# Optimization experiments

Measured on AMD Instinct MI355X. Metric: run time of the kernel, lower is better.

The kernel has to match this reference:

```python
import jax, jax.numpy as jnp
import numpy as np

TOP_K = 2
NORM_MIN = 1e-12
B, S, H = 2, 1024, 2048
E, I = 16, 1024
SHARED_I = 2048  # moe_intermediate_size * moe_num_shared_experts


def setup_inputs() -> dict:
    key = jax.random.key(0)
    ks = jax.random.split(key, 8)
    s = 0.02  # init scale
    return {
        "hidden_states": jax.random.normal(ks[0], (B, S, H), jnp.float32),
        "router_w": jax.random.normal(ks[1], (E, H), jnp.float32) * s,
        "w_gate": jax.random.normal(ks[2], (E, H, I), jnp.float32) * s,
        "w_up": jax.random.normal(ks[3], (E, H, I), jnp.float32) * s,
        "w_down": jax.random.normal(ks[4], (E, I, H), jnp.float32) * s,
        "ws_gate": jax.random.normal(ks[5], (H, SHARED_I), jnp.float32) * s,
        "ws_up": jax.random.normal(ks[6], (H, SHARED_I), jnp.float32) * s,
        "ws_down": jax.random.normal(ks[7], (SHARED_I, H), jnp.float32) * s,
    }


def reference(hidden_states, router_w, w_gate, w_up, w_down, ws_gate, ws_up, ws_down):
    b, s, h = hidden_states.shape
    x = hidden_states.reshape(-1, h)                      # [N, H]
    n = x.shape[0]

    # Router: float32 softmax -> top-k -> renormalize with clamp
    router_logits = x.astype(jnp.float32) @ router_w.T    # [N, E]
    probs = jax.nn.softmax(router_logits, axis=-1)
    rw, sel = jax.lax.top_k(probs, TOP_K)                 # [N, K]
    rw = rw / jnp.clip(rw.sum(axis=-1, keepdims=True), NORM_MIN)
    rw = rw.astype(x.dtype)

    # Dense combine weights [N, E] (equivalent to one_hot dispatch/scatter)
    combine = jnp.zeros((n, E), x.dtype).at[jnp.arange(n)[:, None], sel].set(rw)

    # All-expert SwiGLU MLP (full-capacity MoE, no dropped tokens)
    g = jnp.einsum('nh,ehi->eni', x, w_gate)              # [E, N, I]
    u = jnp.einsum('nh,ehi->eni', x, w_up)
    o = jnp.einsum('eni,eih->enh', jax.nn.silu(g) * u, w_down)  # [E, N, H]
    out = jnp.einsum('enh,ne->nh', o, combine)            # weighted combine

    # Shared expert path
    shared = (jax.nn.silu(x @ ws_gate) * (x @ ws_up)) @ ws_down
    out = out + shared

    return out.reshape(b, s, h), router_logits
```

## Files before the change

### kernel.cpp

```cpp
#include <hip/hip_runtime.h>
#include <cstdint>
#include <cstddef>
#include <cmath>

#define N_TOK 2048
#define HDIM  2048
#define NEXP  16
#define IDIM  1024
#define SIDIM 2048
#define NTHREADS 256

typedef __attribute__((ext_vector_type(8))) short bf16x8;
typedef __attribute__((ext_vector_type(4))) float f32x4;

__device__ __forceinline__ uint32_t f2bf_u(float f) {
    union { float f; uint32_t u; } v; v.f = f;
    return (v.u + 0x7FFFu + ((v.u >> 16) & 1u)) >> 16;
}
__device__ __forceinline__ uint32_t pack2bf(float lo, float hi) {
    return f2bf_u(lo) | (f2bf_u(hi) << 16);
}

__device__ __forceinline__ int swz(int row, int c) {
    return row * 4 + (c ^ ((row >> 1) & 3));
}

__global__ __launch_bounds__(NTHREADS)
void convert_x_kernel(const float* __restrict__ x, unsigned short* __restrict__ xb)
{
    const size_t i = ((size_t)blockIdx.x * NTHREADS + threadIdx.x) * 8;
    float4 a = *(const float4*)(x + i);
    float4 b = *(const float4*)(x + i + 4);
    uint4 w = make_uint4(pack2bf(a.x, a.y), pack2bf(a.z, a.w),
                         pack2bf(b.x, b.y), pack2bf(b.z, b.w));
    *(uint4*)(xb + i) = w;
}

__global__ __launch_bounds__(NTHREADS)
void router_kernel(const float* __restrict__ x,
                   const float* __restrict__ rw,
                   float* __restrict__ logits_out,
                   int* __restrict__ cnt,
                   int* __restrict__ tok_list,
                   float* __restrict__ wt_list)
{
    const int n = blockIdx.x;
    const int tid = threadIdx.x;
    const float* xr = x + (size_t)n * HDIM;

    float acc[NEXP];
#pragma unroll
    for (int e = 0; e < NEXP; ++e) acc[e] = 0.f;

    for (int h = tid; h < HDIM; h += NTHREADS) {
        float xv = xr[h];
#pragma unroll
        for (int e = 0; e < NEXP; ++e) acc[e] += xv * rw[(size_t)e * HDIM + h];
    }

    __shared__ float red[NEXP][NTHREADS];
#pragma unroll
    for (int e = 0; e < NEXP; ++e) red[e][tid] = acc[e];
    __syncthreads();
    for (int s = NTHREADS / 2; s > 0; s >>= 1) {
        if (tid < s) {
#pragma unroll
            for (int e = 0; e < NEXP; ++e) red[e][tid] += red[e][tid + s];
        }
        __syncthreads();
    }

    if (tid < NEXP) logits_out[(size_t)n * NEXP + tid] = red[tid][0];

    if (tid == 0) {
        float l[NEXP];
#pragma unroll
        for (int e = 0; e < NEXP; ++e) l[e] = red[e][0];
        int e0 = 0;
#pragma unroll
        for (int e = 1; e < NEXP; ++e) if (l[e] > l[e0]) e0 = e;
        int e1 = (e0 == 0) ? 1 : 0;
#pragma unroll
        for (int e = 0; e < NEXP; ++e)
            if (e != e0 && l[e] > l[e1]) e1 = e;
        float t = expf(l[e1] - l[e0]);
        float s = 1.f + t;
        float rw0 = 1.f / s;
        float rw1 = t / s;
        int p0 = atomicAdd(&cnt[e0], 1);
        tok_list[e0 * N_TOK + p0] = n;
        wt_list[e0 * N_TOK + p0] = rw0;
        int p1 = atomicAdd(&cnt[e1], 1);
        tok_list[e1 * N_TOK + p1] = n;
        wt_list[e1 * N_TOK + p1] = rw1;
    }
}

__global__ void prefix_kernel(const int* __restrict__ cnt, int* __restrict__ base)
{
    if (threadIdx.x == 0) {
        int s = 0;
        for (int e = 0; e < NEXP; ++e) { base[e] = s; s += cnt[e]; }
    }
}

__global__ __launch_bounds__(NTHREADS)
void dual_swiglu_mfma(const unsigned short* __restrict__ Xb,
                      const float* __restrict__ WgAll,
                      const float* __restrict__ WuAll,
                      unsigned short* __restrict__ Y,
                      const int* __restrict__ cnt,
                      const int* __restrict__ base,
                      const int* __restrict__ tok_list,
                      const int Icols)
{
    const int e  = blockIdx.z;
    const int m0 = blockIdx.y * 128;
    const int n0 = blockIdx.x * 64;
    const bool gathered = (tok_list != nullptr);
    const int M = gathered ? cnt[e] : N_TOK;
    if (m0 >= M) return;
    const float* Wg = WgAll + (size_t)e * HDIM * Icols;
    const float* Wu = WuAll + (size_t)e * HDIM * Icols;
    const int yb = gathered ? base[e] : 0;

    __shared__ short As[128 * 32];
    __shared__ short Gs[64 * 32];
    __shared__ short Us[64 * 32];

    const int tid  = threadIdx.x;
    const int lane = tid & 63;
    const int wave = tid >> 6;
    const int wm   = wave >> 1;
    const int wn   = wave & 1;
    const int l15  = lane & 15;
    const int q    = lane >> 4;

    const int ar = tid >> 1;
    const int at = tid & 1;
    const int slotA = m0 + ar;
    int xrow;
    if (gathered) xrow = tok_list[e * N_TOK + ((slotA < M) ? slotA : (M - 1))];
    else          xrow = slotA;
    const unsigned short* xp = Xb + (size_t)xrow * HDIM + at * 16;

    const int wcn = tid & 63;
    const int wcc = tid >> 6;
    const float* gp = Wg + n0 + wcn;
    const float* up = Wu + n0 + wcn;

    f32x4 accg[4][2], accu[4][2];
#pragma unroll
    for (int i = 0; i < 4; ++i)
#pragma unroll
        for (int j = 0; j < 2; ++j) {
            accg[i][j] = (f32x4){0.f, 0.f, 0.f, 0.f};
            accu[i][j] = (f32x4){0.f, 0.f, 0.f, 0.f};
        }

    uint4 a0, a1;
    float g8[8], u8[8];
    auto ldtile = [&](int kk) {
        a0 = *(const uint4*)(xp + kk);
        a1 = *(const uint4*)(xp + kk + 8);
#pragma unroll
        for (int j = 0; j < 8; ++j) {
            g8[j] = gp[(size_t)(kk + wcc * 8 + j) * Icols];
            u8[j] = up[(size_t)(kk + wcc * 8 + j) * Icols];
        }
    };

    ldtile(0);
    for (int k0 = 0; k0 < HDIM; k0 += 32) {
        __syncthreads();
        *(uint4*)(As + swz(ar, at * 2 + 0) * 8) = a0;
        *(uint4*)(As + swz(ar, at * 2 + 1) * 8) = a1;
        uint4 gw = make_uint4(pack2bf(g8[0], g8[1]), pack2bf(g8[2], g8[3]),
                              pack2bf(g8[4], g8[5]), pack2bf(g8[6], g8[7]));
        uint4 uw = make_uint4(pack2bf(u8[0], u8[1]), pack2bf(u8[2], u8[3]),
                              pack2bf(u8[4], u8[5]), pack2bf(u8[6], u8[7]));
        *(uint4*)(Gs + swz(wcn, wcc) * 8) = gw;
        *(uint4*)(Us + swz(wcn, wcc) * 8) = uw;
        __syncthreads();

        int kn = k0 + 32;
        if (kn >= HDIM) kn = k0;
        ldtile(kn);

        bf16x8 af[4], bg[2], bu[2];
#pragma unroll
        for (int i = 0; i < 4; ++i)
            af[i] = *(const bf16x8*)(As + swz(wm * 64 + i * 16 + l15, q) * 8);
#pragma unroll
        for (int j = 0; j < 2; ++j) {
            bg[j] = *(const bf16x8*)(Gs + swz(wn * 32 + j * 16 + l15, q) * 8);
            bu[j] = *(const bf16x8*)(Us + swz(wn * 32 + j * 16 + l15, q) * 8);
        }
#pragma unroll
        for (int i = 0; i < 4; ++i)
#pragma unroll
            for (int j = 0; j < 2; ++j) {
                accg[i][j] = __builtin_amdgcn_mfma_f32_16x16x32_bf16(af[i], bg[j], accg[i][j], 0, 0, 0);
                accu[i][j] = __builtin_amdgcn_mfma_f32_16x16x32_bf16(af[i], bu[j], accu[i][j], 0, 0, 0);
            }
    }

#pragma unroll
    for (int i = 0; i < 4; ++i) {
#pragma unroll
        for (int r = 0; r < 4; ++r) {
            const int slot = m0 + wm * 64 + i * 16 + q * 4 + r;
            if (slot < M) {
                unsigned short* yrow = Y + (size_t)(yb + slot) * Icols;
#pragma unroll
                for (int j = 0; j < 2; ++j) {
                    const int col = n0 + wn * 32 + j * 16 + l15;
                    float g = accg[i][j][r];
                    float u = accu[i][j][r];
                    float y = (g / (1.f + expf(-g))) * u;
                    yrow[col] = (unsigned short)f2bf_u(y);
                }
            }
        }
    }
}

__global__ __launch_bounds__(NTHREADS)
void down_mfma(const unsigned short* __restrict__ A,
               const float* __restrict__ WdAll,
               float* __restrict__ out,
               const int* __restrict__ cnt,
               const int* __restrict__ base,
               const int* __restrict__ tok_list,
               const float* __restrict__ wt_list,
               const int K)
{
    const int e  = blockIdx.z;
    const int m0 = blockIdx.y * 64;
    const int n0 = blockIdx.x * 128;
    const bool scatter = (tok_list != nullptr);
    const int M = scatter ? cnt[e] : N_TOK;
    if (m0 >= M) return;
    const float* Wd = WdAll + (size_t)e * K * HDIM;
    const int yb = scatter ? base[e] : 0;

    __shared__ short As[64 * 32];
    __shared__ short Bs[128 * 32];

    const int tid  = threadIdx.x;
    const int lane = tid & 63;
    const int wave = tid >> 6;
    const int wm   = wave >> 1;
    const int wn   = wave & 1;
    const int l15  = lane & 15;
    const int q    = lane >> 4;

    const int ar = tid >> 2;
    const int ac = tid & 3;
    const int slotA = m0 + ar;
    const int arow = yb + ((slotA < M) ? slotA : (M - 1));
    const unsigned short* ap = A + (size_t)arow * K + ac * 8;

    const int bn = tid & 127;
    const int bh = tid >> 7;
    const float* bp = Wd + n0 + bn;

    f32x4 acc[2][4];
#pragma unroll
    for (int i = 0; i < 2; ++i)
#pragma unroll
        for (int j = 0; j < 4; ++j) acc[i][j] = (f32x4){0.f, 0.f, 0.f, 0.f};

    uint4 a0;
    float b16[16];
    auto ldtile = [&](int kk) {
        a0 = *(const uint4*)(ap + kk);
#pragma unroll
        for (int c = 0; c < 2; ++c)
#pragma unroll
            for (int j = 0; j < 8; ++j)
                b16[c * 8 + j] = bp[(size_t)(kk + (bh * 2 + c) * 8 + j) * HDIM];
    };

    ldtile(0);
    for (int k0 = 0; k0 < K; k0 += 32) {
        __syncthreads();
        *(uint4*)(As + swz(ar, ac) * 8) = a0;
        uint4 w0 = make_uint4(pack2bf(b16[0], b16[1]), pack2bf(b16[2], b16[3]),
                              pack2bf(b16[4], b16[5]), pack2bf(b16[6], b16[7]));
        uint4 w1 = make_uint4(pack2bf(b16[8], b16[9]), pack2bf(b16[10], b16[11]),
                              pack2bf(b16[12], b16[13]), pack2bf(b16[14], b16[15]));
        *(uint4*)(Bs + swz(bn, bh * 2 + 0) * 8) = w0;
        *(uint4*)(Bs + swz(bn, bh * 2 + 1) * 8) = w1;
        __syncthreads();

        int kn = k0 + 32;
        if (kn >= K) kn = k0;
        ldtile(kn);

        bf16x8 af[2], bfr[4];
#pragma unroll
        for (int i = 0; i < 2; ++i)
            af[i] = *(const bf16x8*)(As + swz(wm * 32 + i * 16 + l15, q) * 8);
#pragma unroll
        for (int j = 0; j < 4; ++j)
            bfr[j] = *(const bf16x8*)(Bs + swz(wn * 64 + j * 16 + l15, q) * 8);
#pragma unroll
        for (int i = 0; i < 2; ++i)
#pragma unroll
            for (int j = 0; j < 4; ++j)
                acc[i][j] = __builtin_amdgcn_mfma_f32_16x16x32_bf16(af[i], bfr[j], acc[i][j], 0, 0, 0);
    }

#pragma unroll
    for (int i = 0; i < 2; ++i) {
#pragma unroll
        for (int r = 0; r < 4; ++r) {
            const int slot = m0 + wm * 32 + i * 16 + q * 4 + r;
            if (slot >= M) continue;
            if (scatter) {
                const int tok = tok_list[e * N_TOK + slot];
                const float wt = wt_list[e * N_TOK + slot];
                float* orow = out + (size_t)tok * HDIM;
#pragma unroll
                for (int j = 0; j < 4; ++j) {
                    const int col = n0 + wn * 64 + j * 16 + l15;
                    atomicAdd(&orow[col], wt * acc[i][j][r]);
                }
            } else {
                float* orow = out + (size_t)slot * HDIM;
#pragma unroll
                for (int j = 0; j < 4; ++j) {
                    const int col = n0 + wn * 64 + j * 16 + l15;
                    orow[col] = acc[i][j][r];
                }
            }
        }
    }
}

extern "C" void kernel_launch(void* const* d_in, const int* in_sizes, int n_in,
                              void* d_out, int out_size, void* d_ws, size_t ws_size,
                              hipStream_t stream)
{
    const float* x       = (const float*)d_in[0];
    const float* rw      = (const float*)d_in[1];
    const float* w_gate  = (const float*)d_in[2];
    const float* w_up    = (const float*)d_in[3];
    const float* w_down  = (const float*)d_in[4];
    const float* ws_gate = (const float*)d_in[5];
    const float* ws_up   = (const float*)d_in[6];
    const float* ws_down = (const float*)d_in[7];

    float* out    = (float*)d_out;
    float* logits = out + (size_t)N_TOK * HDIM;

    char* w = (char*)d_ws;
    int* cnt      = (int*)w;
    int* base     = cnt + 16;
    int* tok_list = base + 16;
    float* wt_list = (float*)(tok_list + NEXP * N_TOK);
    uintptr_t p = (uintptr_t)(wt_list + NEXP * N_TOK);
    p = (p + 255) & ~(uintptr_t)255;
    unsigned short* Xb       = (unsigned short*)p;
    unsigned short* A_shared = Xb + (size_t)N_TOK * HDIM;
    unsigned short* Ybuf     = A_shared + (size_t)N_TOK * SIDIM;

    hipMemsetAsync(cnt, 0, 16 * sizeof(int), stream);

    convert_x_kernel<<<dim3((N_TOK * HDIM) / (NTHREADS * 8)), dim3(NTHREADS), 0, stream>>>(x, Xb);
    router_kernel<<<dim3(N_TOK), dim3(NTHREADS), 0, stream>>>(
        x, rw, logits, cnt, tok_list, wt_list);
    prefix_kernel<<<dim3(1), dim3(64), 0, stream>>>(cnt, base);

    dual_swiglu_mfma<<<dim3(SIDIM / 64, N_TOK / 128, 1), dim3(NTHREADS), 0, stream>>>(
        Xb, ws_gate, ws_up, A_shared, cnt, base, nullptr, SIDIM);
    down_mfma<<<dim3(HDIM / 128, N_TOK / 64, 1), dim3(NTHREADS), 0, stream>>>(
        A_shared, ws_down, out, cnt, base, nullptr, nullptr, SIDIM);

    dual_swiglu_mfma<<<dim3(IDIM / 64, N_TOK / 128, NEXP), dim3(NTHREADS), 0, stream>>>(
        Xb, w_gate, w_up, Ybuf, cnt, base, tok_list, IDIM);
    down_mfma<<<dim3(HDIM / 128, N_TOK / 64, NEXP), dim3(NTHREADS), 0, stream>>>(
        Ybuf, w_down, out, cnt, base, tok_list, wt_list, IDIM);
}
```

Measured before the change: 713.2 us.

## Double-buffer LDS tiles with one barrier per step and hardware bf16 pack

Both the gate/up and down GEMM kernels now keep two LDS buffers and two register tiles. Each k-step issues the global load for the next tile before storing the current one, so there is one barrier per 32-wide k-step instead of two. Float-to-bf16 packing switches from software rounding to the v_cvt_pk_bf16_f32 instruction. The cost is doubled shared memory and more registers, which may reduce occupancy, and the barrier relies on manual waitcnt and sched_barrier ordering.

Measured after the change: 766.3 us. 1.07x slower.

```diff
diff --git a/kernel.cpp b/kernel.cpp
--- a/kernel.cpp
+++ b/kernel.cpp
@@ -17,8 +17,11 @@
     union { float f; uint32_t u; } v; v.f = f;
     return (v.u + 0x7FFFu + ((v.u >> 16) & 1u)) >> 16;
 }
-__device__ __forceinline__ uint32_t pack2bf(float lo, float hi) {
-    return f2bf_u(lo) | (f2bf_u(hi) << 16);
+
+__device__ __forceinline__ uint32_t cvtpk(float lo, float hi) {
+    uint32_t r;
+    asm("v_cvt_pk_bf16_f32 %0, %1, %2" : "=v"(r) : "v"(lo), "v"(hi));
+    return r;
 }
 
 __device__ __forceinline__ int swz(int row, int c) {
@@ -31,8 +34,8 @@
     const size_t i = ((size_t)blockIdx.x * NTHREADS + threadIdx.x) * 8;
     float4 a = *(const float4*)(x + i);
     float4 b = *(const float4*)(x + i + 4);
-    uint4 w = make_uint4(pack2bf(a.x, a.y), pack2bf(a.z, a.w),
-                         pack2bf(b.x, b.y), pack2bf(b.z, b.w));
+    uint4 w = make_uint4(cvtpk(a.x, a.y), cvtpk(a.z, a.w),
+                         cvtpk(b.x, b.y), cvtpk(b.z, b.w));
     *(uint4*)(xb + i) = w;
 }
 
@@ -124,9 +127,9 @@
     const float* Wu = WuAll + (size_t)e * HDIM * Icols;
     const int yb = gathered ? base[e] : 0;
 
-    __shared__ short As[128 * 32];
-    __shared__ short Gs[64 * 32];
-    __shared__ short Us[64 * 32];
+    __shared__ short As[2][128 * 32];
+    __shared__ short Gs[2][64 * 32];
+    __shared__ short Us[2][64 * 32];
 
     const int tid  = threadIdx.x;
     const int lane = tid & 63;
@@ -158,43 +161,39 @@
             accu[i][j] = (f32x4){0.f, 0.f, 0.f, 0.f};
         }
 
-    uint4 a0, a1;
-    float g8[8], u8[8];
-    auto ldtile = [&](int kk) {
-        a0 = *(const uint4*)(xp + kk);
-        a1 = *(const uint4*)(xp + kk + 8);
+    struct RegTile { uint4 x0, x1; float g[8], u[8]; };
+    RegTile r0, r1;
+
+    auto ldtile = [&](RegTile& r, int kk) {
+        r.x0 = *(const uint4*)(xp + kk);
+        r.x1 = *(const uint4*)(xp + kk + 8);
+        const float* gk = gp + (size_t)(kk + wcc * 8) * Icols;
+        const float* uk = up + (size_t)(kk + wcc * 8) * Icols;
 #pragma unroll
         for (int j = 0; j < 8; ++j) {
-            g8[j] = gp[(size_t)(kk + wcc * 8 + j) * Icols];
-            u8[j] = up[(size_t)(kk + wcc * 8 + j) * Icols];
-        }
-    };
-
-    ldtile(0);
-    for (int k0 = 0; k0 < HDIM; k0 += 32) {
-        __syncthreads();
-        *(uint4*)(As + swz(ar, at * 2 + 0) * 8) = a0;
-        *(uint4*)(As + swz(ar, at * 2 + 1) * 8) = a1;
-        uint4 gw = make_uint4(pack2bf(g8[0], g8[1]), pack2bf(g8[2], g8[3]),
-                              pack2bf(g8[4], g8[5]), pack2bf(g8[6], g8[7]));
-        uint4 uw = make_uint4(pack2bf(u8[0], u8[1]), pack2bf(u8[2], u8[3]),
-                              pack2bf(u8[4], u8[5]), pack2bf(u8[6], u8[7]));
-        *(uint4*)(Gs + swz(wcn, wcc) * 8) = gw;
-        *(uint4*)(Us + swz(wcn, wcc) * 8) = uw;
-        __syncthreads();
-
-        int kn = k0 + 32;
-        if (kn >= HDIM) kn = k0;
-        ldtile(kn);
-
+            r.g[j] = gk[(size_t)j * Icols];
+            r.u[j] = uk[(size_t)j * Icols];
+        }
+    };
+    auto sttile = [&](const RegTile& r, short* As_, short* Gs_, short* Us_) {
+        *(uint4*)(As_ + swz(ar, at * 2 + 0) * 8) = r.x0;
+        *(uint4*)(As_ + swz(ar, at * 2 + 1) * 8) = r.x1;
+        uint4 gw = make_uint4(cvtpk(r.g[0], r.g[1]), cvtpk(r.g[2], r.g[3]),
+                              cvtpk(r.g[4], r.g[5]), cvtpk(r.g[6], r.g[7]));
+        uint4 uw = make_uint4(cvtpk(r.u[0], r.u[1]), cvtpk(r.u[2], r.u[3]),
+                              cvtpk(r.u[4], r.u[5]), cvtpk(r.u[6], r.u[7]));
+        *(uint4*)(Gs_ + swz(wcn, wcc) * 8) = gw;
+        *(uint4*)(Us_ + swz(wcn, wcc) * 8) = uw;
+    };
+    auto mmstep = [&](const short* As_, const short* Gs_, const short* Us_) {
         bf16x8 af[4], bg[2], bu[2];
 #pragma unroll
         for (int i = 0; i < 4; ++i)
-            af[i] = *(const bf16x8*)(As + swz(wm * 64 + i * 16 + l15, q) * 8);
+            af[i] = *(const bf16x8*)(As_ + swz(wm * 64 + i * 16 + l15, q) * 8);
 #pragma unroll
         for (int j = 0; j < 2; ++j) {
-            bg[j] = *(const bf16x8*)(Gs + swz(wn * 32 + j * 16 + l15, q) * 8);
-            bu[j] = *(const bf16x8*)(Us + swz(wn * 32 + j * 16 + l15, q) * 8);
+            bg[j] = *(const bf16x8*)(Gs_ + swz(wn * 32 + j * 16 + l15, q) * 8);
+            bu[j] = *(const bf16x8*)(Us_ + swz(wn * 32 + j * 16 + l15, q) * 8);
         }
 #pragma unroll
         for (int i = 0; i < 4; ++i)
@@ -203,6 +202,26 @@
                 accg[i][j] = __builtin_amdgcn_mfma_f32_16x16x32_bf16(af[i], bg[j], accg[i][j], 0, 0, 0);
                 accu[i][j] = __builtin_amdgcn_mfma_f32_16x16x32_bf16(af[i], bu[j], accu[i][j], 0, 0, 0);
             }
+    };
+
+    ldtile(r0, 0);
+    for (int k0 = 0; k0 < HDIM; k0 += 64) {
+        const int k1 = k0 + 32;
+        int k2 = k0 + 64; if (k2 >= HDIM) k2 = 0;
+
+        ldtile(r1, k1);
+        sttile(r0, As[0], Gs[0], Us[0]);
+        asm volatile("s_waitcnt lgkmcnt(0)" ::: "memory");
+        __builtin_amdgcn_s_barrier();
+        __builtin_amdgcn_sched_barrier(0);
+        mmstep(As[0], Gs[0], Us[0]);
+
+        ldtile(r0, k2);
+        sttile(r1, As[1], Gs[1], Us[1]);
+        asm volatile("s_waitcnt lgkmcnt(0)" ::: "memory");
+        __builtin_amdgcn_s_barrier();
+        __builtin_amdgcn_sched_barrier(0);
+        mmstep(As[1], Gs[1], Us[1]);
     }
 
 #pragma unroll
@@ -244,8 +263,8 @@
     const float* Wd = WdAll + (size_t)e * K * HDIM;
     const int yb = scatter ? base[e] : 0;
 
-    __shared__ short As[64 * 32];
-    __shared__ short Bs[128 * 32];
+    __shared__ short As[2][64 * 32];
+    __shared__ short Bs[2][128 * 32];
 
     const int tid  = threadIdx.x;
     const int lane = tid & 63;
@@ -271,45 +290,60 @@
 #pragma unroll
         for (int j = 0; j < 4; ++j) acc[i][j] = (f32x4){0.f, 0.f, 0.f, 0.f};
 
-    uint4 a0;
-    float b16[16];
-    auto ldtile = [&](int kk) {
-        a0 = *(const uint4*)(ap + kk);
+    struct RegTileD { uint4 x; float b[16]; };
+    RegTileD r0, r1;
+
+    auto ldtile = [&](RegTileD& r, int kk) {
+        r.x = *(const uint4*)(ap + kk);
+        const float* bk = bp + (size_t)(kk + bh * 16) * HDIM;
 #pragma unroll
         for (int c = 0; c < 2; ++c)
 #pragma unroll
             for (int j = 0; j < 8; ++j)
-                b16[c * 8 + j] = bp[(size_t)(kk + (bh * 2 + c) * 8 + j) * HDIM];
-    };
-
-    ldtile(0);
-    for (int k0 = 0; k0 < K; k0 += 32) {
-        __syncthreads();
-        *(uint4*)(As + swz(ar, ac) * 8) = a0;
-        uint4 w0 = make_uint4(pack2bf(b16[0], b16[1]), pack2bf(b16[2], b16[3]),
-                              pack2bf(b16[4], b16[5]), pack2bf(b16[6], b16[7]));
-        uint4 w1 = make_uint4(pack2bf(b16[8], b16[9]), pack2bf(b16[10], b16[11]),
-                              pack2bf(b16[12], b16[13]), pack2bf(b16[14], b16[15]));
-        *(uint4*)(Bs + swz(bn, bh * 2 + 0) * 8) = w0;
-        *(uint4*)(Bs + swz(bn, bh * 2 + 1) * 8) = w1;
-        __syncthreads();
-
-        int kn = k0 + 32;
-        if (kn >= K) kn = k0;
-        ldtile(kn);
-
+                r.b[c * 8 + j] = bk[(size_t)(c * 8 + j) * HDIM];
+    };
+    auto sttile = [&](const RegTileD& r, short* As_, short* Bs_) {
+        *(uint4*)(As_ + swz(ar, ac) * 8) = r.x;
+        uint4 w0 = make_uint4(cvtpk(r.b[0], r.b[1]),  cvtpk(r.b[2], r.b[3]),
+                              cvtpk(r.b[4], r.b[5]),  cvtpk(r.b[6], r.b[7]));
+        uint4 w1 = make_uint4(cvtpk(r.b[8], r.b[9]),  cvtpk(r.b[10], r.b[11]),
+                              cvtpk(r.b[12], r.b[13]), cvtpk(r.b[14], r.b[15]));
+        *(uint4*)(Bs_ + swz(bn, bh * 2 + 0) * 8) = w0;
+        *(uint4*)(Bs_ + swz(bn, bh * 2 + 1) * 8) = w1;
+    };
+    auto mmstep = [&](const short* As_, const short* Bs_) {
         bf16x8 af[2], bfr[4];
 #pragma unroll
         for (int i = 0; i < 2; ++i)
-            af[i] = *(const bf16x8*)(As + swz(wm * 32 + i * 16 + l15, q) * 8);
+            af[i] = *(const bf16x8*)(As_ + swz(wm * 32 + i * 16 + l15, q) * 8);
 #pragma unroll
         for (int j = 0; j < 4; ++j)
-            bfr[j] = *(const bf16x8*)(Bs + swz(wn * 64 + j * 16 + l15, q) * 8);
+            bfr[j] = *(const bf16x8*)(Bs_ + swz(wn * 64 + j * 16 + l15, q) * 8);
 #pragma unroll
         for (int i = 0; i < 2; ++i)
 #pragma unroll
             for (int j = 0; j < 4; ++j)
                 acc[i][j] = __builtin_amdgcn_mfma_f32_16x16x32_bf16(af[i], bfr[j], acc[i][j], 0, 0, 0);
+    };
+
+    ldtile(r0, 0);
+    for (int k0 = 0; k0 < K; k0 += 64) {
+        const int k1 = k0 + 32;
+        int k2 = k0 + 64; if (k2 >= K) k2 = 0;
+
+        ldtile(r1, k1);
+        sttile(r0, As[0], Bs[0]);
+        asm volatile("s_waitcnt lgkmcnt(0)" ::: "memory");
+        __builtin_amdgcn_s_barrier();
+        __builtin_amdgcn_sched_barrier(0);
+        mmstep(As[0], Bs[0]);
+
+        ldtile(r0, k2);
+        sttile(r1, As[1], Bs[1]);
+        asm volatile("s_waitcnt lgkmcnt(0)" ::: "memory");
+        __builtin_amdgcn_s_barrier();
+        __builtin_amdgcn_sched_barrier(0);
+        mmstep(As[1], Bs[1]);
     }
 
 #pragma unroll
```

## Merge shared and routed expert GEMMs into single launches; use hardware bf16 pack

Applied to the files above, without the earlier changes.

Folds the shared-expert GEMMs into the routed-expert launches as an extra z-slice, so the up/gate and down stages each run as one grid instead of two. The down stage now accumulates the shared path with atomics too, which requires zeroing the output with a memset first. Float-to-bf16 packing now uses the v_cvt_pk_bf16_f32 instruction instead of manual rounding. The aim is fewer launches, better GPU fill from the small sparse grids, and cheaper conversion. In exchange, the shared path pays atomic traffic and a full output memset, and many blocks exit early in the padded grid.

After: 756.4 us. 1.06x slower.

```diff
diff --git a/kernel.cpp b/kernel.cpp
--- a/kernel.cpp
+++ b/kernel.cpp
@@ -17,8 +17,11 @@
     union { float f; uint32_t u; } v; v.f = f;
     return (v.u + 0x7FFFu + ((v.u >> 16) & 1u)) >> 16;
 }
-__device__ __forceinline__ uint32_t pack2bf(float lo, float hi) {
-    return f2bf_u(lo) | (f2bf_u(hi) << 16);
+
+__device__ __forceinline__ uint32_t cvtpk(float lo, float hi) {
+    uint32_t r;
+    asm("v_cvt_pk_bf16_f32 %0, %1, %2" : "=v"(r) : "v"(lo), "v"(hi));
+    return r;
 }
 
 __device__ __forceinline__ int swz(int row, int c) {
@@ -31,8 +34,8 @@
     const size_t i = ((size_t)blockIdx.x * NTHREADS + threadIdx.x) * 8;
     float4 a = *(const float4*)(x + i);
     float4 b = *(const float4*)(x + i + 4);
-    uint4 w = make_uint4(pack2bf(a.x, a.y), pack2bf(a.z, a.w),
-                         pack2bf(b.x, b.y), pack2bf(b.z, b.w));
+    uint4 w = make_uint4(cvtpk(a.x, a.y), cvtpk(a.z, a.w),
+                         cvtpk(b.x, b.y), cvtpk(b.z, b.w));
     *(uint4*)(xb + i) = w;
 }
 
@@ -108,21 +111,27 @@
 void dual_swiglu_mfma(const unsigned short* __restrict__ Xb,
                       const float* __restrict__ WgAll,
                       const float* __restrict__ WuAll,
-                      unsigned short* __restrict__ Y,
+                      const float* __restrict__ Wsg,
+                      const float* __restrict__ Wsu,
+                      unsigned short* __restrict__ Ysparse,
+                      unsigned short* __restrict__ Yshared,
                       const int* __restrict__ cnt,
                       const int* __restrict__ base,
-                      const int* __restrict__ tok_list,
-                      const int Icols)
-{
-    const int e  = blockIdx.z;
+                      const int* __restrict__ tok_list)
+{
+    const int z  = blockIdx.z;
+    const bool shared_path = (z == 0);
+    const int e  = z - 1;
+    const int Icols = shared_path ? SIDIM : IDIM;
     const int m0 = blockIdx.y * 128;
     const int n0 = blockIdx.x * 64;
-    const bool gathered = (tok_list != nullptr);
-    const int M = gathered ? cnt[e] : N_TOK;
+    if (n0 >= Icols) return;
+    const int M = shared_path ? N_TOK : cnt[e];
     if (m0 >= M) return;
-    const float* Wg = WgAll + (size_t)e * HDIM * Icols;
-    const float* Wu = WuAll + (size_t)e * HDIM * Icols;
-    const int yb = gathered ? base[e] : 0;
+    const float* Wg = shared_path ? Wsg : WgAll + (size_t)e * HDIM * IDIM;
+    const float* Wu = shared_path ? Wsu : WuAll + (size_t)e * HDIM * IDIM;
+    unsigned short* Y = shared_path ? Yshared : Ysparse;
+    const int yb = shared_path ? 0 : base[e];
 
     __shared__ short As[128 * 32];
     __shared__ short Gs[64 * 32];
@@ -140,8 +149,8 @@
     const int at = tid & 1;
     const int slotA = m0 + ar;
     int xrow;
-    if (gathered) xrow = tok_list[e * N_TOK + ((slotA < M) ? slotA : (M - 1))];
-    else          xrow = slotA;
+    if (!shared_path) xrow = tok_list[e * N_TOK + ((slotA < M) ? slotA : (M - 1))];
+    else              xrow = slotA;
     const unsigned short* xp = Xb + (size_t)xrow * HDIM + at * 16;
 
     const int wcn = tid & 63;
@@ -175,10 +184,10 @@
         __syncthreads();
         *(uint4*)(As + swz(ar, at * 2 + 0) * 8) = a0;
         *(uint4*)(As + swz(ar, at * 2 + 1) * 8) = a1;
-        uint4 gw = make_uint4(pack2bf(g8[0], g8[1]), pack2bf(g8[2], g8[3]),
-                              pack2bf(g8[4], g8[5]), pack2bf(g8[6], g8[7]));
-        uint4 uw = make_uint4(pack2bf(u8[0], u8[1]), pack2bf(u8[2], u8[3]),
-                              pack2bf(u8[4], u8[5]), pack2bf(u8[6], u8[7]));
+        uint4 gw = make_uint4(cvtpk(g8[0], g8[1]), cvtpk(g8[2], g8[3]),
+                              cvtpk(g8[4], g8[5]), cvtpk(g8[6], g8[7]));
+        uint4 uw = make_uint4(cvtpk(u8[0], u8[1]), cvtpk(u8[2], u8[3]),
+                              cvtpk(u8[4], u8[5]), cvtpk(u8[6], u8[7]));
         *(uint4*)(Gs + swz(wcn, wcc) * 8) = gw;
         *(uint4*)(Us + swz(wcn, wcc) * 8) = uw;
         __syncthreads();
@@ -226,23 +235,27 @@
 }
 
 __global__ __launch_bounds__(NTHREADS)
-void down_mfma(const unsigned short* __restrict__ A,
+void down_mfma(const unsigned short* __restrict__ Ash,
+               const unsigned short* __restrict__ Asp,
+               const float* __restrict__ Wsd,
                const float* __restrict__ WdAll,
                float* __restrict__ out,
                const int* __restrict__ cnt,
                const int* __restrict__ base,
                const int* __restrict__ tok_list,
-               const float* __restrict__ wt_list,
-               const int K)
-{
-    const int e  = blockIdx.z;
+               const float* __restrict__ wt_list)
+{
+    const int z  = blockIdx.z;
+    const bool shared_path = (z == 0);
+    const int e  = z - 1;
+    const int K  = shared_path ? SIDIM : IDIM;
     const int m0 = blockIdx.y * 64;
     const int n0 = blockIdx.x * 128;
-    const bool scatter = (tok_list != nullptr);
-    const int M = scatter ? cnt[e] : N_TOK;
+    const int M = shared_path ? N_TOK : cnt[e];
     if (m0 >= M) return;
-    const float* Wd = WdAll + (size_t)e * K * HDIM;
-    const int yb = scatter ? base[e] : 0;
+    const unsigned short* A = shared_path ? Ash : Asp;
+    const float* Wd = shared_path ? Wsd : WdAll + (size_t)e * IDIM * HDIM;
+    const int yb = shared_path ? 0 : base[e];
 
     __shared__ short As[64 * 32];
     __shared__ short Bs[128 * 32];
@@ -286,10 +299,10 @@
     for (int k0 = 0; k0 < K; k0 += 32) {
         __syncthreads();
         *(uint4*)(As + swz(ar, ac) * 8) = a0;
-        uint4 w0 = make_uint4(pack2bf(b16[0], b16[1]), pack2bf(b16[2], b16[3]),
-                              pack2bf(b16[4], b16[5]), pack2bf(b16[6], b16[7]));
-        uint4 w1 = make_uint4(pack2bf(b16[8], b16[9]), pack2bf(b16[10], b16[11]),
-                              pack2bf(b16[12], b16[13]), pack2bf(b16[14], b16[15]));
+        uint4 w0 = make_uint4(cvtpk(b16[0], b16[1]),  cvtpk(b16[2], b16[3]),
+                              cvtpk(b16[4], b16[5]),  cvtpk(b16[6], b16[7]));
+        uint4 w1 = make_uint4(cvtpk(b16[8], b16[9]),  cvtpk(b16[10], b16[11]),
+                              cvtpk(b16[12], b16[13]), cvtpk(b16[14], b16[15]));
         *(uint4*)(Bs + swz(bn, bh * 2 + 0) * 8) = w0;
         *(uint4*)(Bs + swz(bn, bh * 2 + 1) * 8) = w1;
         __syncthreads();
@@ -318,22 +331,13 @@
         for (int r = 0; r < 4; ++r) {
             const int slot = m0 + wm * 32 + i * 16 + q * 4 + r;
             if (slot >= M) continue;
-            if (scatter) {
-                const int tok = tok_list[e * N_TOK + slot];
-                const float wt = wt_list[e * N_TOK + slot];
-                float* orow = out + (size_t)tok * HDIM;
-#pragma unroll
-                for (int j = 0; j < 4; ++j) {
-                    const int col = n0 + wn * 64 + j * 16 + l15;
-                    atomicAdd(&orow[col], wt * acc[i][j][r]);
-                }
-            } else {
-                float* orow = out + (size_t)slot * HDIM;
-#pragma unroll
-                for (int j = 0; j < 4; ++j) {
-                    const int col = n0 + wn * 64 + j * 16 + l15;
-                    orow[col] = acc[i][j][r];
-                }
+            const int tok  = shared_path ? slot : tok_list[e * N_TOK + slot];
+            const float wt = shared_path ? 1.f  : wt_list[e * N_TOK + slot];
+            float* orow = out + (size_t)tok * HDIM;
+#pragma unroll
+            for (int j = 0; j < 4; ++j) {
+                const int col = n0 + wn * 64 + j * 16 + l15;
+                atomicAdd(&orow[col], wt * acc[i][j][r]);
             }
         }
     }
@@ -367,19 +371,16 @@
     unsigned short* Ybuf     = A_shared + (size_t)N_TOK * SIDIM;
 
     hipMemsetAsync(cnt, 0, 16 * sizeof(int), stream);
+    hipMemsetAsync(out, 0, (size_t)N_TOK * HDIM * sizeof(float), stream);
 
     convert_x_kernel<<<dim3((N_TOK * HDIM) / (NTHREADS * 8)), dim3(NTHREADS), 0, stream>>>(x, Xb);
     router_kernel<<<dim3(N_TOK), dim3(NTHREADS), 0, stream>>>(
         x, rw, logits, cnt, tok_list, wt_list);
     prefix_kernel<<<dim3(1), dim3(64), 0, stream>>>(cnt, base);
 
-    dual_swiglu_mfma<<<dim3(SIDIM / 64, N_TOK / 128, 1), dim3(NTHREADS), 0, stream>>>(
-        Xb, ws_gate, ws_up, A_shared, cnt, base, nullptr, SIDIM);
-    down_mfma<<<dim3(HDIM / 128, N_TOK / 64, 1), dim3(NTHREADS), 0, stream>>>(
-        A_shared, ws_down, out, cnt, base, nullptr, nullptr, SIDIM);
-
-    dual_swiglu_mfma<<<dim3(IDIM / 64, N_TOK / 128, NEXP), dim3(NTHREADS), 0, stream>>>(
-        Xb, w_gate, w_up, Ybuf, cnt, base, tok_list, IDIM);
-    down_mfma<<<dim3(HDIM / 128, N_TOK / 64, NEXP), dim3(NTHREADS), 0, stream>>>(
-        Ybuf, w_down, out, cnt, base, tok_list, wt_list, IDIM);
-}
+    dual_swiglu_mfma<<<dim3(SIDIM / 64, N_TOK / 128, NEXP + 1), dim3(NTHREADS), 0, stream>>>(
+        Xb, w_gate, w_up, ws_gate, ws_up, Ybuf, A_shared, cnt, base, tok_list);
+
+    down_mfma<<<dim3(HDIM / 128, N_TOK / 64, NEXP + 1), dim3(NTHREADS), 0, stream>>>(
+        A_shared, Ybuf, ws_down, w_down, out, cnt, base, tok_list, wt_list);
+}
```
